# Performance work log

Measured on AMD Instinct MI355X. Metric: run time of the kernel, lower is better.

Reference implementation:

```python
import jax, jax.numpy as jnp
import numpy as np

TEMPERATURE = 30.0
NUM_KERNELS = 4


def setup_inputs() -> dict:
    key = jax.random.key(0)
    ks = jax.random.split(key, 7)
    B, H, W, C = 32, 56, 56, 256
    F, KH, KW, K = 256, 3, 3, NUM_KERNELS
    hidden = C // 4  # attention_reduction_ratio = 4
    x = jax.random.normal(ks[0], (B, H, W, C), dtype=jnp.float32)
    # K parallel conv kernels (HWIO layout) and biases
    fan = KH * KW * C
    kernels = jax.random.normal(ks[1], (K, KH, KW, C, F), dtype=jnp.float32) / np.sqrt(fan)
    biases = jnp.zeros((K, F), dtype=jnp.float32)
    # attention MLP: GAP -> Dense(C//4, relu) -> Dense(K)
    w1 = jax.random.normal(ks[2], (C, hidden), dtype=jnp.float32) / np.sqrt(C)
    b1 = jnp.zeros((hidden,), dtype=jnp.float32)
    w2 = jax.random.normal(ks[3], (hidden, K), dtype=jnp.float32) / np.sqrt(hidden)
    b2 = jnp.zeros((K,), dtype=jnp.float32)
    return {"x": x, "kernels": kernels, "biases": biases,
            "w1": w1, "b1": b1, "w2": w2, "b2": b2}


def reference(x, kernels, biases, w1, b1, w2, b2):
    # Attention router: GAP -> Dense(relu) -> Dense(K) -> softmax(logits / tau)
    pooled = jnp.mean(x, axis=(1, 2))                       # [B, C]
    h = jax.nn.relu(pooled @ w1 + b1)                       # [B, C//4]
    logits = h @ w2 + b2                                    # [B, K]
    attn = jax.nn.softmax(logits / TEMPERATURE, axis=-1)    # [B, K]

    # K parallel conv branches (stride 1, SAME padding, dilation 1, groups 1)
    def conv_k(w, b):
        y = jax.lax.conv_general_dilated(
            x, w, window_strides=(1, 1), padding='SAME',
            dimension_numbers=('NHWC', 'HWIO', 'NHWC'))
        return y + b                                        # [B, H, W, F]

    ys = jax.vmap(conv_k)(kernels, biases)                  # [K, B, H, W, F]
    # per-sample weighted aggregation of branch outputs
    out = jnp.einsum('kbhwf,bk->bhwf', ys, attn)            # [B, H, W, F]
    return out
```

## Files before the change

### kernel.cpp

```cpp
#include <hip/hip_runtime.h>
#include <hip/hip_bf16.h>
#include <stdint.h>

typedef __bf16 bf16_t;
typedef __bf16 bf16x4 __attribute__((ext_vector_type(4)));
typedef __bf16 bf16x8 __attribute__((ext_vector_type(8)));
typedef float floatx4 __attribute__((ext_vector_type(4)));

#define B_ 32
#define HP 58
#define WP 66

#define XPAD_OFF   0u
#define WAGG_OFF   62717952u
#define POOLED_OFF 100466688u
#define ATTN_OFF   100499456u
#define BIASAGG_OFF 100499968u

__device__ __forceinline__ void async_copy16(const void* gsrc, void* ldst) {
  __builtin_amdgcn_global_load_lds(
      (const __attribute__((address_space(1))) unsigned int*)gsrc,
      (__attribute__((address_space(3))) unsigned int*)ldst, 16, 0, 0);
}

__global__ __launch_bounds__(256)
void pad_pool(const float* __restrict__ x, bf16_t* __restrict__ xpad,
              float* __restrict__ pooled) {
  const int hp = blockIdx.x;
  const int b  = blockIdx.y;
  const int t  = threadIdx.x;
  const int c4 = (t & 63) << 2;
  const int wq = t >> 6;
  const int h  = hp - 1;
  const bool hvalid = (h >= 0) && (h < 56);
  bf16_t* dst = xpad + ((size_t)(b * 58 + hp)) * (66 * 256);
  const float* srcrow = x + ((size_t)(b * 56 + (hvalid ? h : 0))) * (56 * 256);
  floatx4 sum = {0.f, 0.f, 0.f, 0.f};
  for (int wp = wq; wp < 66; wp += 4) {
    const int w = wp - 1;
    floatx4 v = {0.f, 0.f, 0.f, 0.f};
    if (hvalid && (unsigned)w < 56u) {
      v = *(const floatx4*)(srcrow + w * 256 + c4);
      sum += v;
    }
    bf16x4 r;
#pragma unroll
    for (int j = 0; j < 4; ++j) r[j] = (bf16_t)v[j];
    *(bf16x4*)(dst + wp * 256 + c4) = r;
  }
  __shared__ floatx4 red[4][64];
  red[wq][t & 63] = sum;
  __syncthreads();
  if (hvalid && t < 64) {
    floatx4 s = red[0][t] + red[1][t] + red[2][t] + red[3][t];
#pragma unroll
    for (int j = 0; j < 4; ++j) atomicAdd(&pooled[b * 256 + t * 4 + j], s[j]);
  }
}

__global__ __launch_bounds__(256)
void router(const float* __restrict__ pooled, const float* __restrict__ w1,
            const float* __restrict__ b1, const float* __restrict__ w2,
            const float* __restrict__ b2, const float* __restrict__ biases,
            float* __restrict__ attn, float* __restrict__ biasagg) {
  __shared__ float ps[8192];
  __shared__ float w1s[16384];
  __shared__ float hs[2048];
  __shared__ float lg[128];
  __shared__ float at[128];
  const int t = threadIdx.x;
  for (int i = t; i < 8192; i += 256) ps[i] = pooled[i] * (1.0f / 3136.0f);
  for (int i = t; i < 4096; i += 256)
    *(floatx4*)&w1s[i * 4] = *(const floatx4*)&w1[i * 4];
  __syncthreads();
  for (int task = t; task < 2048; task += 256) {
    const int b = task >> 6, j = task & 63;
    const float* pb = ps + b * 256;
    float s0 = 0.f, s1 = 0.f, s2 = 0.f, s3 = 0.f;
#pragma unroll 4
    for (int c = 0; c < 256; c += 4) {
      s0 += pb[c]     * w1s[c * 64 + j];
      s1 += pb[c + 1] * w1s[(c + 1) * 64 + j];
      s2 += pb[c + 2] * w1s[(c + 2) * 64 + j];
      s3 += pb[c + 3] * w1s[(c + 3) * 64 + j];
    }
    hs[task] = fmaxf((s0 + s1) + (s2 + s3) + b1[j], 0.f);
  }
  __syncthreads();
  if (t < 128) {
    int b = t >> 2, k = t & 3;
    float s = b2[k];
    const float* hb = hs + b * 64;
#pragma unroll 4
    for (int j = 0; j < 64; ++j) s += hb[j] * w2[j * 4 + k];
    lg[t] = s * (1.0f / 30.0f);
  }
  __syncthreads();
  if (t < 32) {
    int b = t;
    float z0 = lg[b*4], z1 = lg[b*4+1], z2 = lg[b*4+2], z3 = lg[b*4+3];
    float m = fmaxf(fmaxf(z0, z1), fmaxf(z2, z3));
    float e0 = expf(z0-m), e1 = expf(z1-m), e2 = expf(z2-m), e3 = expf(z3-m);
    float inv = 1.0f / (e0 + e1 + e2 + e3);
    at[b*4] = e0*inv; at[b*4+1] = e1*inv; at[b*4+2] = e2*inv; at[b*4+3] = e3*inv;
    attn[b*4] = at[b*4]; attn[b*4+1] = at[b*4+1];
    attn[b*4+2] = at[b*4+2]; attn[b*4+3] = at[b*4+3];
  }
  __syncthreads();
  for (int i = t; i < 8192; i += 256) {
    int b = i >> 8, f = i & 255;
    biasagg[i] = at[b*4]*biases[f] + at[b*4+1]*biases[256+f]
               + at[b*4+2]*biases[512+f] + at[b*4+3]*biases[768+f];
  }
}

__global__ __launch_bounds__(256)
void wagg_kernel(const float* __restrict__ kers, const float* __restrict__ attn,
                 bf16_t* __restrict__ wagg) {
  const int lid = blockIdx.x;
  const int xcd = lid & 7;
  const int sl  = lid >> 3;
  const int c8  = sl & 7;
  const int tap = sl >> 3;
  const int b0  = xcd << 2;
  const int t   = threadIdx.x;
  __shared__ bf16_t tile[4][32 * 260];

  float a[4][4];
#pragma unroll
  for (int i = 0; i < 4; ++i)
#pragma unroll
    for (int k = 0; k < 4; ++k) a[i][k] = attn[(b0 + i) * 4 + k];

  const float* k0 = kers + ((size_t)(0 * 9 + tap)) * 65536 + (size_t)(c8 * 32) * 256;
  const float* k1 = kers + ((size_t)(1 * 9 + tap)) * 65536 + (size_t)(c8 * 32) * 256;
  const float* k2 = kers + ((size_t)(2 * 9 + tap)) * 65536 + (size_t)(c8 * 32) * 256;
  const float* k3 = kers + ((size_t)(3 * 9 + tap)) * 65536 + (size_t)(c8 * 32) * 256;

  const int fq = t & 63;
  const int cl = t >> 6;
  const int f0 = fq * 4;
#pragma unroll
  for (int pass = 0; pass < 8; ++pass) {
    const int c_local = pass * 4 + cl;
    const size_t o = (size_t)c_local * 256 + f0;
    floatx4 v0 = *(const floatx4*)(k0 + o);
    floatx4 v1 = *(const floatx4*)(k1 + o);
    floatx4 v2 = *(const floatx4*)(k2 + o);
    floatx4 v3 = *(const floatx4*)(k3 + o);
#pragma unroll
    for (int i = 0; i < 4; ++i) {
      bf16x4 r;
#pragma unroll
      for (int j = 0; j < 4; ++j)
        r[j] = (bf16_t)(a[i][0] * v0[j] + a[i][1] * v1[j] + a[i][2] * v2[j] + a[i][3] * v3[j]);
      *(bf16x4*)&tile[i][c_local * 260 + f0] = r;
    }
  }
  __syncthreads();

#pragma unroll
  for (int i = 0; i < 4; ++i) {
    bf16_t* wt = wagg + ((size_t)((b0 + i) * 9 + tap)) * 65536 + c8 * 32;
#pragma unroll
    for (int pass = 0; pass < 4; ++pass) {
      const int gi = pass * 256 + t;
      const int f  = gi >> 2;
      const int cg = gi & 3;
      bf16x8 v;
#pragma unroll
      for (int jj = 0; jj < 8; ++jj) v[jj] = tile[i][(cg * 8 + jj) * 260 + f];
      *(bf16x8*)(wt + (size_t)f * 256 + cg * 8) = v;
    }
  }
}

#define PBUF_BYTES 20480
#define BBUF_BYTES 16384

__global__ __launch_bounds__(256, 2)
void conv_mfma(const bf16_t* __restrict__ xpad, const bf16_t* __restrict__ wagg,
               const float* __restrict__ biasagg, float* __restrict__ out) {
  __shared__ char lds[PBUF_BYTES + 3 * BBUF_BYTES];
  char* ldsP = lds;
  char* ldsB = lds + PBUF_BYTES;

  const int lid  = blockIdx.y * 28 + blockIdx.x;
  const int nid  = (lid & 7) * 112 + (lid >> 3);
  const int b    = nid / 28;
  const int tile = nid - b * 28;
  const int h0 = (tile >> 2) * 8;
  const int w0 = (tile & 3) * 14;

  const int tid  = threadIdx.x;
  const int lane = tid & 63;
  const int wv   = tid >> 6;
  const int l15  = lane & 15;
  const int quad = lane >> 4;
  const int n0   = wv * 64;

  const char* xb = (const char*)xpad + (size_t)b * (HP * WP * 256 * 2);
  const char* wb = (const char*)wagg + (size_t)b * (9 * 256 * 256 * 2);

  int offs[7];
#pragma unroll
  for (int mi = 0; mi < 7; ++mi) {
    int m = mi * 16 + l15;
    int ty = m / 14;
    int tx = m - ty * 14;
    offs[mi] = ty * 16 + tx;
  }
  int boff[4];
#pragma unroll
  for (int ni = 0; ni < 4; ++ni) {
    int f = n0 + ni * 16 + l15;
    boff[ni] = f * 64 + ((quad ^ ((f >> 1) & 3)) << 4);
  }
  int sb_off[4], sb_lds[4];
#pragma unroll
  for (int ii = 0; ii < 4; ++ii) {
    int i16 = wv * 4 + ii;
    int f = i16 * 16 + (lane >> 2);
    int gsrc = (lane & 3) ^ ((f >> 1) & 3);
    sb_off[ii] = f * 512 + gsrc * 16;
    sb_lds[ii] = i16 * 1024;
  }
  int sp_off[5], sp_lds[5];
#pragma unroll
  for (int ii = 0; ii < 5; ++ii) {
    int i20 = wv * 5 + ii;
    int p = i20 * 8 + (lane >> 3);
    int gsrc = (lane & 7) ^ (p & 7);
    sp_off[ii] = ((h0 + (p >> 4)) * WP + (w0 + (p & 15))) * 512 + gsrc * 16;
    sp_lds[ii] = i20 * 1024;
  }

  floatx4 acc[7][4];
#pragma unroll
  for (int mi = 0; mi < 7; ++mi)
#pragma unroll
    for (int ni = 0; ni < 4; ++ni) acc[mi][ni] = (floatx4){0.f, 0.f, 0.f, 0.f};

  auto stage_patch = [&](int cq) {
#pragma unroll
    for (int ii = 0; ii < 5; ++ii)
      async_copy16(xb + cq * 128 + sp_off[ii], ldsP + sp_lds[ii]);
  };
  auto stage_b = [&](int tap, int kbyte, int slot) {
    const char* wtb = wb + (size_t)tap * 131072 + kbyte;
#pragma unroll
    for (int ii = 0; ii < 4; ++ii)
      async_copy16(wtb + sb_off[ii], ldsB + slot * BBUF_BYTES + sb_lds[ii]);
  };

  stage_patch(0);
  stage_b(0, 0, 0);

  bf16x8 aA[7], aB[7];
  int aoff[7];
  int slot = 0;

#pragma unroll 1
  for (int d = 0; d < 36; ++d) {
    const int cq  = d / 9;
    const int tap = d - cq * 9;
    const int s1 = (slot == 2) ? 0 : slot + 1;
    const int s2 = (s1 == 2) ? 0 : s1 + 1;

    stage_b(tap, cq * 128 + 64, s1);
    asm volatile("s_waitcnt vmcnt(4)" ::: "memory");
    __builtin_amdgcn_s_barrier();
    __builtin_amdgcn_sched_barrier(0);
    {
      const char* bc = ldsB + slot * BBUF_BYTES;
      bf16x8 bv0 = *(const bf16x8*)(bc + boff[0]);
      bf16x8 bv1 = *(const bf16x8*)(bc + boff[1]);
      bf16x8 bv2 = *(const bf16x8*)(bc + boff[2]);
      bf16x8 bv3 = *(const bf16x8*)(bc + boff[3]);
      if (tap == 0) {
        const int tapoff = 0;
#pragma unroll
        for (int mi = 0; mi < 7; ++mi) {
          int p = offs[mi] + tapoff;
          aoff[mi] = (p << 7) + ((quad ^ (p & 7)) << 4);
          aA[mi] = *(const bf16x8*)(ldsP + aoff[mi]);
        }
      }
#pragma unroll
      for (int mi = 0; mi < 7; ++mi)
        aB[mi] = *(const bf16x8*)(ldsP + (aoff[mi] ^ 64));
      __builtin_amdgcn_s_setprio(1);
#pragma unroll
      for (int mi = 0; mi < 7; ++mi) {
        acc[mi][0] = __builtin_amdgcn_mfma_f32_16x16x32_bf16(aA[mi], bv0, acc[mi][0], 0, 0, 0);
        acc[mi][1] = __builtin_amdgcn_mfma_f32_16x16x32_bf16(aA[mi], bv1, acc[mi][1], 0, 0, 0);
        acc[mi][2] = __builtin_amdgcn_mfma_f32_16x16x32_bf16(aA[mi], bv2, acc[mi][2], 0, 0, 0);
        acc[mi][3] = __builtin_amdgcn_mfma_f32_16x16x32_bf16(aA[mi], bv3, acc[mi][3], 0, 0, 0);
      }
      __builtin_amdgcn_s_setprio(0);
    }

    const bool last = (d == 35);
    if (!last) {
      const int ntap = (tap == 8) ? 0 : tap + 1;
      const int ncq  = (tap == 8) ? cq + 1 : cq;
      stage_b(ntap, ncq * 128, s2);
      asm volatile("s_waitcnt vmcnt(4)" ::: "memory");
    } else {
      asm volatile("s_waitcnt vmcnt(0)" ::: "memory");
    }
    __builtin_amdgcn_s_barrier();
    __builtin_amdgcn_sched_barrier(0);
    {
      const char* bc = ldsB + s1 * BBUF_BYTES;
      bf16x8 bv0 = *(const bf16x8*)(bc + boff[0]);
      bf16x8 bv1 = *(const bf16x8*)(bc + boff[1]);
      bf16x8 bv2 = *(const bf16x8*)(bc + boff[2]);
      bf16x8 bv3 = *(const bf16x8*)(bc + boff[3]);
      __builtin_amdgcn_s_setprio(1);
#pragma unroll
      for (int mi = 0; mi < 7; ++mi) {
        acc[mi][0] = __builtin_amdgcn_mfma_f32_16x16x32_bf16(aB[mi], bv0, acc[mi][0], 0, 0, 0);
        acc[mi][1] = __builtin_amdgcn_mfma_f32_16x16x32_bf16(aB[mi], bv1, acc[mi][1], 0, 0, 0);
        acc[mi][2] = __builtin_amdgcn_mfma_f32_16x16x32_bf16(aB[mi], bv2, acc[mi][2], 0, 0, 0);
        acc[mi][3] = __builtin_amdgcn_mfma_f32_16x16x32_bf16(aB[mi], bv3, acc[mi][3], 0, 0, 0);
      }
      __builtin_amdgcn_s_setprio(0);
      if (tap < 8) {
        const int ntapoff = ((tap + 1) / 3) * 16 + ((tap + 1) % 3);
#pragma unroll
        for (int mi = 0; mi < 7; ++mi) {
          int p = offs[mi] + ntapoff;
          aoff[mi] = (p << 7) + ((quad ^ (p & 7)) << 4);
          aA[mi] = *(const bf16x8*)(ldsP + aoff[mi]);
        }
      } else if (!last) {
        __builtin_amdgcn_s_barrier();
        stage_patch(cq + 1);
      }
    }
    slot = s2;
  }

  float bias[4];
#pragma unroll
  for (int ni = 0; ni < 4; ++ni) bias[ni] = biasagg[b * 256 + n0 + ni * 16 + l15];
  float* outb = out + (size_t)b * (56 * 56 * 256);
#pragma unroll
  for (int mi = 0; mi < 7; ++mi) {
#pragma unroll
    for (int rg = 0; rg < 4; ++rg) {
      int m = mi * 16 + quad * 4 + rg;
      int ty = m / 14, tx = m - ty * 14;
      float* orow = outb + ((size_t)((h0 + ty) * 56) + (w0 + tx)) * 256 + n0 + l15;
#pragma unroll
      for (int ni = 0; ni < 4; ++ni) orow[ni * 16] = acc[mi][ni][rg] + bias[ni];
    }
  }
}

extern "C" void kernel_launch(void* const* d_in, const int* in_sizes, int n_in,
                              void* d_out, int out_size, void* d_ws, size_t ws_size,
                              hipStream_t stream) {
  const float* x      = (const float*)d_in[0];
  const float* kers   = (const float*)d_in[1];
  const float* biases = (const float*)d_in[2];
  const float* w1     = (const float*)d_in[3];
  const float* b1     = (const float*)d_in[4];
  const float* w2     = (const float*)d_in[5];
  const float* b2     = (const float*)d_in[6];
  float* outp = (float*)d_out;
  char* ws = (char*)d_ws;

  bf16_t* xpad   = (bf16_t*)(ws + XPAD_OFF);
  bf16_t* wagg   = (bf16_t*)(ws + WAGG_OFF);
  float* pooled  = (float*)(ws + POOLED_OFF);
  float* attn    = (float*)(ws + ATTN_OFF);
  float* biasagg = (float*)(ws + BIASAGG_OFF);

  hipMemsetAsync(pooled, 0, 32 * 256 * sizeof(float), stream);
  pad_pool<<<dim3(58, 32), 256, 0, stream>>>(x, xpad, pooled);
  router<<<1, 256, 0, stream>>>(pooled, w1, b1, w2, b2, biases, attn, biasagg);
  wagg_kernel<<<dim3(576), 256, 0, stream>>>(kers, attn, wagg);
  conv_mfma<<<dim3(28, 32), 256, 0, stream>>>(xpad, wagg, biasagg, outp);
}
```

Before: 371.7 us.

## Enlarge conv tile to 8x28 with 512-thread blocks and K=64 weight staging

Each conv block now covers twice the spatial width (8x28 pixels) using 8 waves: two M-groups share the same staged weight tile across four filter slices. Weight stages grow to 64 channels per slot, giving one barrier per tap instead of two. This halves global weight traffic per output pixel and reduces synchronization count. In exchange it raises LDS use to roughly 136 KB per block, which likely limits residency to one block per CU, and it halves the grid size.

```diff
diff --git a/kernel.cpp b/kernel.cpp
--- a/kernel.cpp
+++ b/kernel.cpp
@@ -175,29 +175,31 @@
   }
 }
 
-#define PBUF_BYTES 20480
-#define BBUF_BYTES 16384
-
-__global__ __launch_bounds__(256, 2)
+#define PBUF_BYTES 40960
+#define BBUF_BYTES 32768
+
+__global__ __launch_bounds__(512, 2)
 void conv_mfma(const bf16_t* __restrict__ xpad, const bf16_t* __restrict__ wagg,
                const float* __restrict__ biasagg, float* __restrict__ out) {
   __shared__ char lds[PBUF_BYTES + 3 * BBUF_BYTES];
   char* ldsP = lds;
   char* ldsB = lds + PBUF_BYTES;
 
-  const int lid  = blockIdx.y * 28 + blockIdx.x;
-  const int nid  = (lid & 7) * 112 + (lid >> 3);
-  const int b    = nid / 28;
-  const int tile = nid - b * 28;
-  const int h0 = (tile >> 2) * 8;
-  const int w0 = (tile & 3) * 14;
+  const int lid  = blockIdx.y * 14 + blockIdx.x;
+  const int nid  = (lid & 7) * 56 + (lid >> 3);
+  const int b    = nid / 14;
+  const int tile = nid - b * 14;
+  const int h0 = (tile >> 1) * 8;
+  const int w0 = (tile & 1) * 28;
 
   const int tid  = threadIdx.x;
   const int lane = tid & 63;
   const int wv   = tid >> 6;
+  const int mg   = wv >> 2;
+  const int fs   = wv & 3;
   const int l15  = lane & 15;
   const int quad = lane >> 4;
-  const int n0   = wv * 64;
+  const int n0   = fs * 64;
 
   const char* xb = (const char*)xpad + (size_t)b * (HP * WP * 256 * 2);
   const char* wb = (const char*)wagg + (size_t)b * (9 * 256 * 256 * 2);
@@ -205,34 +207,33 @@
   int offs[7];
 #pragma unroll
   for (int mi = 0; mi < 7; ++mi) {
-    int m = mi * 16 + l15;
-    int ty = m / 14;
-    int tx = m - ty * 14;
-    offs[mi] = ty * 16 + tx;
+    int m = mg * 112 + mi * 16 + l15;
+    int ty = m / 28;
+    int tx = m - ty * 28;
+    offs[mi] = ty * 32 + tx;
   }
   int boff[4];
 #pragma unroll
   for (int ni = 0; ni < 4; ++ni) {
     int f = n0 + ni * 16 + l15;
-    boff[ni] = f * 64 + ((quad ^ ((f >> 1) & 3)) << 4);
-  }
-  int sb_off[4], sb_lds[4];
+    boff[ni] = f * 128 + ((quad ^ (f & 7)) << 4);
+  }
+  int sb_off[4];
 #pragma unroll
   for (int ii = 0; ii < 4; ++ii) {
-    int i16 = wv * 4 + ii;
-    int f = i16 * 16 + (lane >> 2);
-    int gsrc = (lane & 3) ^ ((f >> 1) & 3);
+    int i32 = wv * 4 + ii;
+    int f = i32 * 8 + (lane >> 3);
+    int gsrc = (lane & 7) ^ (f & 7);
     sb_off[ii] = f * 512 + gsrc * 16;
-    sb_lds[ii] = i16 * 1024;
-  }
-  int sp_off[5], sp_lds[5];
+  }
+  int sp_off[5];
 #pragma unroll
   for (int ii = 0; ii < 5; ++ii) {
-    int i20 = wv * 5 + ii;
-    int p = i20 * 8 + (lane >> 3);
+    int i40 = wv * 5 + ii;
+    int p = i40 * 8 + (lane >> 3);
+    int row = p >> 5, col = p & 31;
     int gsrc = (lane & 7) ^ (p & 7);
-    sp_off[ii] = ((h0 + (p >> 4)) * WP + (w0 + (p & 15))) * 512 + gsrc * 16;
-    sp_lds[ii] = i20 * 1024;
+    sp_off[ii] = ((h0 + row) * WP + (w0 + col)) * 512 + gsrc * 16;
   }
 
   floatx4 acc[7][4];
@@ -244,13 +245,13 @@
   auto stage_patch = [&](int cq) {
 #pragma unroll
     for (int ii = 0; ii < 5; ++ii)
-      async_copy16(xb + cq * 128 + sp_off[ii], ldsP + sp_lds[ii]);
+      async_copy16(xb + cq * 128 + sp_off[ii], ldsP + (wv * 5 + ii) * 1024);
   };
-  auto stage_b = [&](int tap, int kbyte, int slot) {
-    const char* wtb = wb + (size_t)tap * 131072 + kbyte;
+  auto stage_b = [&](int tap, int cq, int slot) {
+    const char* wtb = wb + (size_t)tap * 131072 + cq * 128;
 #pragma unroll
     for (int ii = 0; ii < 4; ++ii)
-      async_copy16(wtb + sb_off[ii], ldsB + slot * BBUF_BYTES + sb_lds[ii]);
+      async_copy16(wtb + sb_off[ii], ldsB + slot * BBUF_BYTES + (wv * 4 + ii) * 1024);
   };
 
   stage_patch(0);
@@ -265,81 +266,73 @@
     const int cq  = d / 9;
     const int tap = d - cq * 9;
     const int s1 = (slot == 2) ? 0 : slot + 1;
-    const int s2 = (s1 == 2) ? 0 : s1 + 1;
-
-    stage_b(tap, cq * 128 + 64, s1);
-    asm volatile("s_waitcnt vmcnt(4)" ::: "memory");
-    __builtin_amdgcn_s_barrier();
-    __builtin_amdgcn_sched_barrier(0);
-    {
-      const char* bc = ldsB + slot * BBUF_BYTES;
-      bf16x8 bv0 = *(const bf16x8*)(bc + boff[0]);
-      bf16x8 bv1 = *(const bf16x8*)(bc + boff[1]);
-      bf16x8 bv2 = *(const bf16x8*)(bc + boff[2]);
-      bf16x8 bv3 = *(const bf16x8*)(bc + boff[3]);
-      if (tap == 0) {
-        const int tapoff = 0;
-#pragma unroll
-        for (int mi = 0; mi < 7; ++mi) {
-          int p = offs[mi] + tapoff;
-          aoff[mi] = (p << 7) + ((quad ^ (p & 7)) << 4);
-          aA[mi] = *(const bf16x8*)(ldsP + aoff[mi]);
-        }
-      }
-#pragma unroll
-      for (int mi = 0; mi < 7; ++mi)
-        aB[mi] = *(const bf16x8*)(ldsP + (aoff[mi] ^ 64));
-      __builtin_amdgcn_s_setprio(1);
-#pragma unroll
-      for (int mi = 0; mi < 7; ++mi) {
-        acc[mi][0] = __builtin_amdgcn_mfma_f32_16x16x32_bf16(aA[mi], bv0, acc[mi][0], 0, 0, 0);
-        acc[mi][1] = __builtin_amdgcn_mfma_f32_16x16x32_bf16(aA[mi], bv1, acc[mi][1], 0, 0, 0);
-        acc[mi][2] = __builtin_amdgcn_mfma_f32_16x16x32_bf16(aA[mi], bv2, acc[mi][2], 0, 0, 0);
-        acc[mi][3] = __builtin_amdgcn_mfma_f32_16x16x32_bf16(aA[mi], bv3, acc[mi][3], 0, 0, 0);
-      }
-      __builtin_amdgcn_s_setprio(0);
-    }
-
     const bool last = (d == 35);
+
     if (!last) {
-      const int ntap = (tap == 8) ? 0 : tap + 1;
-      const int ncq  = (tap == 8) ? cq + 1 : cq;
-      stage_b(ntap, ncq * 128, s2);
+      const int nt = (tap == 8) ? 0 : tap + 1;
+      const int nc = (tap == 8) ? cq + 1 : cq;
+      stage_b(nt, nc, s1);
       asm volatile("s_waitcnt vmcnt(4)" ::: "memory");
     } else {
       asm volatile("s_waitcnt vmcnt(0)" ::: "memory");
     }
     __builtin_amdgcn_s_barrier();
     __builtin_amdgcn_sched_barrier(0);
-    {
-      const char* bc = ldsB + s1 * BBUF_BYTES;
-      bf16x8 bv0 = *(const bf16x8*)(bc + boff[0]);
-      bf16x8 bv1 = *(const bf16x8*)(bc + boff[1]);
-      bf16x8 bv2 = *(const bf16x8*)(bc + boff[2]);
-      bf16x8 bv3 = *(const bf16x8*)(bc + boff[3]);
-      __builtin_amdgcn_s_setprio(1);
+
+    const char* bc = ldsB + slot * BBUF_BYTES;
+    bf16x8 bv0 = *(const bf16x8*)(bc + boff[0]);
+    bf16x8 bv1 = *(const bf16x8*)(bc + boff[1]);
+    bf16x8 bv2 = *(const bf16x8*)(bc + boff[2]);
+    bf16x8 bv3 = *(const bf16x8*)(bc + boff[3]);
+    if (tap == 0) {
 #pragma unroll
       for (int mi = 0; mi < 7; ++mi) {
-        acc[mi][0] = __builtin_amdgcn_mfma_f32_16x16x32_bf16(aB[mi], bv0, acc[mi][0], 0, 0, 0);
-        acc[mi][1] = __builtin_amdgcn_mfma_f32_16x16x32_bf16(aB[mi], bv1, acc[mi][1], 0, 0, 0);
-        acc[mi][2] = __builtin_amdgcn_mfma_f32_16x16x32_bf16(aB[mi], bv2, acc[mi][2], 0, 0, 0);
-        acc[mi][3] = __builtin_amdgcn_mfma_f32_16x16x32_bf16(aB[mi], bv3, acc[mi][3], 0, 0, 0);
+        int p = offs[mi];
+        aoff[mi] = (p << 7) + ((quad ^ (p & 7)) << 4);
+        aA[mi] = *(const bf16x8*)(ldsP + aoff[mi]);
       }
-      __builtin_amdgcn_s_setprio(0);
-      if (tap < 8) {
-        const int ntapoff = ((tap + 1) / 3) * 16 + ((tap + 1) % 3);
-#pragma unroll
-        for (int mi = 0; mi < 7; ++mi) {
-          int p = offs[mi] + ntapoff;
-          aoff[mi] = (p << 7) + ((quad ^ (p & 7)) << 4);
-          aA[mi] = *(const bf16x8*)(ldsP + aoff[mi]);
-        }
-      } else if (!last) {
-        __builtin_amdgcn_s_barrier();
-        stage_patch(cq + 1);
+    }
+    __builtin_amdgcn_s_setprio(1);
+#pragma unroll
+    for (int mi = 0; mi < 7; ++mi) {
+      acc[mi][0] = __builtin_amdgcn_mfma_f32_16x16x32_bf16(aA[mi], bv0, acc[mi][0], 0, 0, 0);
+      acc[mi][1] = __builtin_amdgcn_mfma_f32_16x16x32_bf16(aA[mi], bv1, acc[mi][1], 0, 0, 0);
+      acc[mi][2] = __builtin_amdgcn_mfma_f32_16x16x32_bf16(aA[mi], bv2, acc[mi][2], 0, 0, 0);
+      acc[mi][3] = __builtin_amdgcn_mfma_f32_16x16x32_bf16(aA[mi], bv3, acc[mi][3], 0, 0, 0);
+    }
+    __builtin_amdgcn_s_setprio(0);
+
+    bf16x8 cv0 = *(const bf16x8*)(bc + (boff[0] ^ 64));
+    bf16x8 cv1 = *(const bf16x8*)(bc + (boff[1] ^ 64));
+    bf16x8 cv2 = *(const bf16x8*)(bc + (boff[2] ^ 64));
+    bf16x8 cv3 = *(const bf16x8*)(bc + (boff[3] ^ 64));
+#pragma unroll
+    for (int mi = 0; mi < 7; ++mi)
+      aB[mi] = *(const bf16x8*)(ldsP + (aoff[mi] ^ 64));
+    if (tap < 8) {
+      const int ntapoff = ((tap + 1) / 3) * 32 + ((tap + 1) % 3);
+#pragma unroll
+      for (int mi = 0; mi < 7; ++mi) {
+        int p = offs[mi] + ntapoff;
+        aoff[mi] = (p << 7) + ((quad ^ (p & 7)) << 4);
+        aA[mi] = *(const bf16x8*)(ldsP + aoff[mi]);
       }
     }
-    slot = s2;
+    __builtin_amdgcn_s_setprio(1);
+#pragma unroll
+    for (int mi = 0; mi < 7; ++mi) {
+      acc[mi][0] = __builtin_amdgcn_mfma_f32_16x16x32_bf16(aB[mi], cv0, acc[mi][0], 0, 0, 0);
+      acc[mi][1] = __builtin_amdgcn_mfma_f32_16x16x32_bf16(aB[mi], cv1, acc[mi][1], 0, 0, 0);
+      acc[mi][2] = __builtin_amdgcn_mfma_f32_16x16x32_bf16(aB[mi], cv2, acc[mi][2], 0, 0, 0);
+      acc[mi][3] = __builtin_amdgcn_mfma_f32_16x16x32_bf16(aB[mi], cv3, acc[mi][3], 0, 0, 0);
+    }
+    __builtin_amdgcn_s_setprio(0);
+
+    if (tap == 8 && cq < 3) {
+      __builtin_amdgcn_s_barrier();
+      stage_patch(cq + 1);
+    }
+    slot = s1;
   }
 
   float bias[4];
@@ -350,8 +343,8 @@
   for (int mi = 0; mi < 7; ++mi) {
 #pragma unroll
     for (int rg = 0; rg < 4; ++rg) {
-      int m = mi * 16 + quad * 4 + rg;
-      int ty = m / 14, tx = m - ty * 14;
+      int m = mg * 112 + mi * 16 + quad * 4 + rg;
+      int ty = m / 28, tx = m - ty * 28;
       float* orow = outb + ((size_t)((h0 + ty) * 56) + (w0 + tx)) * 256 + n0 + l15;
 #pragma unroll
       for (int ni = 0; ni < 4; ++ni) orow[ni * 16] = acc[mi][ni][rg] + bias[ni];
@@ -382,5 +375,5 @@
   pad_pool<<<dim3(58, 32), 256, 0, stream>>>(x, xpad, pooled);
   router<<<1, 256, 0, stream>>>(pooled, w1, b1, w2, b2, biases, attn, biasagg);
   wagg_kernel<<<dim3(576), 256, 0, stream>>>(kers, attn, wagg);
-  conv_mfma<<<dim3(28, 32), 256, 0, stream>>>(xpad, wagg, biasagg, outp);
-}
+  conv_mfma<<<dim3(14, 32), 512, 0, stream>>>(xpad, wagg, biasagg, outp);
+}
```

Result: faster. 361.8 us (-2.7%).
